# Performance work log

Hardware: AMD Instinct MI355X
Metric: run time of the kernel (lower is better)

The kernel has to match this reference:

```python
import jax, jax.numpy as jnp
import numpy as np

B, N, C_IN, T = 16, 1024, 16, 36
K, C_OUT = 3, 64


def setup_inputs() -> dict:
    key = jax.random.key(0)
    k1, k2, k3, k4 = jax.random.split(key, 4)
    x = jax.random.normal(k1, (B, N, C_IN, T), dtype=jnp.float32)
    spatial_attention = jax.random.uniform(k2, (B, N, N), dtype=jnp.float32)
    cheb = jax.random.normal(k3, (K, N, N), dtype=jnp.float32) * 0.1
    theta = jax.random.normal(k4, (K, C_IN, C_OUT), dtype=jnp.float32) * 0.1
    return {"x": x, "spatial_attention": spatial_attention, "cheb": cheb, "theta": theta}


def reference(x, spatial_attention, cheb, theta):
    # x: [B,N,C_in,T], spatial_attention: [B,N,N], cheb: [K,N,N], theta: [K,C_in,C_out]
    # Original: per (t,k): ((T_k * SAt).T @ x[..., t]) @ theta_k, summed over k, ReLU.
    # Compute attention-weighted adjacency ONCE (time-invariant), batch over all t.
    t_at = cheb[:, None, :, :] * spatial_attention[None]          # [K,B,N,N]
    # rhs[k,b,n,c,t] = sum_m t_at[k,b,m,n] * x[b,m,c,t]  (permute(0,2,1).matmul)
    rhs = jnp.einsum('kbmn,bmct->kbnct', t_at, x)                 # [K,B,N,C_in,T]
    out = jnp.einsum('kbnct,kco->bnot', rhs, theta)               # [B,N,C_out,T]
    return jax.nn.relu(out)
```

## Files before the change

kernel.cpp:

```cpp
#include <hip/hip_runtime.h>
#include <hip/hip_bf16.h>

#define NB 16
#define NN 1024
#define CIN 16
#define TT 36
#define KK 3
#define COUT 64
#define CT 576
#define KB 48

typedef __attribute__((ext_vector_type(8))) short bf16x8;
typedef __attribute__((ext_vector_type(4))) float f32x4;

__device__ __forceinline__ unsigned short f2bf(float f) {
    union { float f; unsigned int u; } v; v.f = f;
    unsigned int r = v.u + 0x7FFF + ((v.u >> 16) & 1);
    return (unsigned short)(r >> 16);
}

__global__ __launch_bounds__(256) void prep_a(const float* __restrict__ cheb,
                                              const float* __restrict__ sat,
                                              ushort* __restrict__ At,
                                              int n_base, int rows) {
    __shared__ ushort tile[64][68];
    const int ntiles = rows >> 6;
    const int k = blockIdx.y;
    const int n0 = n_base + (blockIdx.x % ntiles) * 64;
    const int m0 = (blockIdx.x / ntiles) * 64;
    const int tid = threadIdx.x;

    size_t goff[4];
    float4 cv[4], sv[4];
#pragma unroll
    for (int i = 0; i < 4; ++i) {
        int f = i * 256 + tid;
        goff[i] = (size_t)(m0 + (f >> 4)) * NN + n0 + ((f & 15) << 2);
        cv[i] = *(const float4*)(cheb + (size_t)k * NN * NN + goff[i]);
        sv[i] = *(const float4*)(sat + goff[i]);
    }
    for (int b = 0; b < 16; ++b) {
#pragma unroll
        for (int i = 0; i < 4; ++i) {
            int f = i * 256 + tid;
            ushort4 u;
            u.x = f2bf(cv[i].x * sv[i].x); u.y = f2bf(cv[i].y * sv[i].y);
            u.z = f2bf(cv[i].z * sv[i].z); u.w = f2bf(cv[i].w * sv[i].w);
            *(ushort4*)&tile[f >> 4][(f & 15) << 2] = u;
        }
        if (b < 15) {
            const float* sa = sat + (size_t)(b + 1) * NN * NN;
#pragma unroll
            for (int i = 0; i < 4; ++i) sv[i] = *(const float4*)(sa + goff[i]);
        }
        __syncthreads();
        ushort* outp = At + (size_t)(k * 16 + b) * rows * NN;
#pragma unroll
        for (int i = 0; i < 4; ++i) {
            int f = i * 256 + tid;
            int n = f >> 4, m4 = (f & 15) << 2;
            ushort4 u;
            u.x = tile[m4 + 0][n]; u.y = tile[m4 + 1][n];
            u.z = tile[m4 + 2][n]; u.w = tile[m4 + 3][n];
            *(ushort4*)(outp + (size_t)(n0 - n_base + n) * NN + m0 + m4) = u;
        }
        __syncthreads();
    }
}

__global__ __launch_bounds__(256) void prep_x(const float* __restrict__ x,
                                              ushort* __restrict__ Xt) {
    __shared__ ushort tile[64][68];
    const int b = blockIdx.y;
    const int m0 = (blockIdx.x & 15) * 64;
    const int c0 = (blockIdx.x >> 4) * 64;
    const int tid = threadIdx.x;
    const float* xb = x + (size_t)b * NN * CT;
#pragma unroll
    for (int i = 0; i < 4; ++i) {
        int f = i * 256 + tid;
        int mr = f >> 4, c4 = (f & 15) << 2;
        float4 v = *(const float4*)(xb + (size_t)(m0 + mr) * CT + c0 + c4);
        ushort4 u;
        u.x = f2bf(v.x); u.y = f2bf(v.y); u.z = f2bf(v.z); u.w = f2bf(v.w);
        *(ushort4*)&tile[mr][c4] = u;
    }
    __syncthreads();
    ushort* outp = Xt + (size_t)b * CT * NN;
#pragma unroll
    for (int i = 0; i < 4; ++i) {
        int f = i * 256 + tid;
        int n = f >> 4, m4 = (f & 15) << 2;
        int ctlin = c0 + n;
        int c = ctlin / 36, t = ctlin - 36 * c;
        int ctp = t * 16 + c;
        ushort4 u;
        u.x = tile[m4 + 0][n]; u.y = tile[m4 + 1][n];
        u.z = tile[m4 + 2][n]; u.w = tile[m4 + 3][n];
        *(ushort4*)(outp + (size_t)ctp * NN + m0 + m4) = u;
    }
}

__global__ __launch_bounds__(512) void gemm1(const ushort* __restrict__ At,
                                             const ushort* __restrict__ Xt,
                                             ushort* __restrict__ rhs2,
                                             int nsplit, int n_base, int rows) {
    __shared__ ushort lds[3 * 320 * 64];
    const int tid = threadIdx.x;
    const int y = blockIdx.y;
    const int b = y / 3, k = y - 3 * b;
    const int l = k * 16 + b;
    const int ntiles = rows >> 7;
    const int nt = blockIdx.x % ntiles;
    const int ctt = blockIdx.x / ntiles;
    const int nloc0 = nt * 128;
    const int ct0 = ctt * 192;
    const ushort* Ab = At + ((size_t)l * (nsplit ? rows : NN) + nloc0) * NN;
    const ushort* Bb = Xt + (size_t)b * CT * NN + (size_t)ct0 * NN;

    const int srow = tid >> 3;
    const int schunk = tid & 7;
    const int swz = schunk ^ (srow & 7);
    const ushort* a_src0 = Ab + (size_t)srow * NN + swz * 8;
    const ushort* b_src0 = Bb + (size_t)srow * NN + swz * 8;

    auto STAGE = [&](int kt, int p) {
        const int mk = kt * 64;
        ushort* base = lds + p * (320 * 64);
        const ushort* as = a_src0 + mk;
        const ushort* bs = b_src0 + mk;
#pragma unroll
        for (int i = 0; i < 2; ++i)
            __builtin_amdgcn_global_load_lds(
                (const __attribute__((address_space(1))) void*)(as + (size_t)i * 64 * NN),
                (__attribute__((address_space(3))) void*)(base + (tid + i * 512) * 8), 16, 0, 0);
#pragma unroll
        for (int i = 0; i < 3; ++i)
            __builtin_amdgcn_global_load_lds(
                (const __attribute__((address_space(1))) void*)(bs + (size_t)i * 64 * NN),
                (__attribute__((address_space(3))) void*)(base + 128 * 64 + (tid + i * 512) * 8), 16, 0, 0);
    };

    const int w = tid >> 6, lane = tid & 63;
    const int wr = w >> 2, wc = w & 3;
    const int lrow = lane & 15, quad = lane >> 4;
    const int koff0 = ((quad ^ (lrow & 7)) << 3);
    f32x4 acc[4][3] = {};

    STAGE(0, 0);
    STAGE(1, 1);
    asm volatile("s_waitcnt vmcnt(5)\n\ts_barrier" ::: "memory");

    for (int kt = 0; kt < 16; ++kt) {
        if (kt + 2 < 16)
            STAGE(kt + 2, (kt + 2) % 3);
        const ushort* bufA = lds + (kt % 3) * (320 * 64);
        const ushort* bufB = bufA + 128 * 64;
#pragma unroll
        for (int kp = 0; kp < 2; ++kp) {
            const int koff = koff0 ^ (kp << 5);
            bf16x8 af[4], bfr[3];
#pragma unroll
            for (int mi = 0; mi < 4; ++mi)
                af[mi] = *(const bf16x8*)&bufA[(wr * 64 + mi * 16 + lrow) * 64 + koff];
#pragma unroll
            for (int ni = 0; ni < 3; ++ni)
                bfr[ni] = *(const bf16x8*)&bufB[(wc * 48 + ni * 16 + lrow) * 64 + koff];
            __builtin_amdgcn_s_setprio(1);
#pragma unroll
            for (int mi = 0; mi < 4; ++mi)
#pragma unroll
                for (int ni = 0; ni < 3; ++ni)
                    acc[mi][ni] = __builtin_amdgcn_mfma_f32_16x16x32_bf16(
                        af[mi], bfr[ni], acc[mi][ni], 0, 0, 0);
            __builtin_amdgcn_s_setprio(0);
        }
        if (kt + 2 < 16)
            asm volatile("s_waitcnt vmcnt(5)\n\ts_barrier" ::: "memory");
        else if (kt + 1 < 16)
            asm volatile("s_waitcnt vmcnt(0)\n\ts_barrier" ::: "memory");
        else
            asm volatile("s_barrier" ::: "memory");
    }

    ushort* cs = lds;
#pragma unroll
    for (int mi = 0; mi < 4; ++mi)
#pragma unroll
        for (int ni = 0; ni < 3; ++ni)
#pragma unroll
            for (int r = 0; r < 4; ++r)
                cs[(wr * 64 + mi * 16 + quad * 4 + r) * 200 + wc * 48 + ni * 16 + lrow] =
                    f2bf(acc[mi][ni][r]);
    __syncthreads();

    for (int f = tid; f < 1536; f += 512) {
        int n = f / 12, tl = f - 12 * (f / 12);
        int t = ctt * 12 + tl;
        uint4 v0 = *(const uint4*)&cs[n * 200 + tl * 16];
        uint4 v1 = *(const uint4*)&cs[n * 200 + tl * 16 + 8];
        size_t g = (((size_t)b * NN + n_base + nloc0 + n) * 36 + t) * 48 + k * 16;
        *(uint4*)(rhs2 + g) = v0;
        *(uint4*)(rhs2 + g + 8) = v1;
    }
}

__global__ __launch_bounds__(256) void apply_mfma2(const ushort* __restrict__ rhs2,
                                                   const float* __restrict__ theta,
                                                   float* __restrict__ out) {
    __shared__ ushort thT[64 * 72];
    __shared__ float ostage[4][64 * 36];
    const int tid = threadIdx.x;
    for (int f = tid; f < 64 * 64; f += 256) {
        int o = f >> 6, kc = f & 63;
        thT[o * 72 + kc] = f2bf((kc < 48) ? theta[kc * 64 + o] : 0.f);
    }
    __syncthreads();
    const int w = tid >> 6, lane = tid & 63;
    const int lrow = lane & 15, quad = lane >> 4;

    bf16x8 a[4][2];
#pragma unroll
    for (int mi = 0; mi < 4; ++mi)
#pragma unroll
        for (int kc = 0; kc < 2; ++kc)
            a[mi][kc] = *(const bf16x8*)&thT[(mi * 16 + lrow) * 72 + kc * 32 + quad * 8];

    float* ost = &ostage[w][0];
    for (int j = 0; j < 4; ++j) {
        const int bn = blockIdx.x * 16 + w * 4 + j;
        const ushort* rrow = rhs2 + (size_t)bn * (36 * 48);
        f32x4 acc[4][3] = {};
#pragma unroll
        for (int ni = 0; ni < 3; ++ni)
#pragma unroll
            for (int kc = 0; kc < 2; ++kc) {
                bf16x8 bf = *(const bf16x8*)(rrow + (ni * 16 + lrow) * 48 + kc * 32 + quad * 8);
#pragma unroll
                for (int mi = 0; mi < 4; ++mi)
                    acc[mi][ni] = __builtin_amdgcn_mfma_f32_16x16x32_bf16(
                        a[mi][kc], bf, acc[mi][ni], 0, 0, 0);
            }
#pragma unroll
        for (int mi = 0; mi < 4; ++mi)
#pragma unroll
            for (int ni = 0; ni < 3; ++ni)
#pragma unroll
                for (int r = 0; r < 4; ++r) {
                    int t = ni * 16 + lrow;
                    if (t < 36)
                        ost[(mi * 16 + quad * 4 + r) * 36 + t] = fmaxf(acc[mi][ni][r], 0.f);
                }
        asm volatile("s_waitcnt lgkmcnt(0)" ::: "memory");
        float* ob = out + (size_t)bn * (COUT * TT);
#pragma unroll
        for (int q = 0; q < 9; ++q) {
            int f = q * 64 + lane;
            *(float4*)&ob[f * 4] = *(const float4*)&ost[f * 4];
        }
    }
}

__global__ __launch_bounds__(256) void naive_fused(const float* __restrict__ x,
                                                   const float* __restrict__ sat,
                                                   const float* __restrict__ cheb,
                                                   const float* __restrict__ theta,
                                                   float* __restrict__ out) {
    __shared__ float wgt[3][1024];
    __shared__ float rs[3][576];
    const int tid = threadIdx.x;
    const int n = blockIdx.x, b = blockIdx.y;
    for (int f = tid; f < 3 * 1024; f += 256) {
        int k = f >> 10, m = f & 1023;
        wgt[k][m] = cheb[(size_t)k * NN * NN + (size_t)m * NN + n] *
                    sat[(size_t)b * NN * NN + (size_t)m * NN + n];
    }
    __syncthreads();
    float a0[3] = {}, a1[3] = {}, a2[3] = {};
    const float* xb = x + (size_t)b * NN * CT;
    for (int m = 0; m < 1024; ++m) {
        const float* xr = xb + (size_t)m * CT;
        float x0 = xr[tid];
        float x1 = xr[256 + tid];
        float x2 = (tid < 64) ? xr[512 + tid] : 0.f;
#pragma unroll
        for (int k = 0; k < 3; ++k) {
            float wm = wgt[k][m];
            a0[k] += wm * x0; a1[k] += wm * x1; a2[k] += wm * x2;
        }
    }
#pragma unroll
    for (int k = 0; k < 3; ++k) {
        rs[k][tid] = a0[k];
        rs[k][256 + tid] = a1[k];
        if (tid < 64) rs[k][512 + tid] = a2[k];
    }
    __syncthreads();
    const int o = tid >> 2, tg = tid & 3;
    float oa[9] = {};
    for (int kc = 0; kc < 48; ++kc) {
        int k = kc >> 4, c = kc & 15;
        float th = theta[kc * 64 + o];
        const float* rp = &rs[k][c * TT + tg * 9];
#pragma unroll
        for (int j = 0; j < 9; ++j) oa[j] += th * rp[j];
    }
    float* ob = out + ((size_t)b * NN + n) * (COUT * TT);
#pragma unroll
    for (int j = 0; j < 9; ++j)
        ob[o * TT + tg * 9 + j] = fmaxf(oa[j], 0.f);
}

extern "C" void kernel_launch(void* const* d_in, const int* in_sizes, int n_in,
                              void* d_out, int out_size, void* d_ws, size_t ws_size,
                              hipStream_t stream) {
    const float* x     = (const float*)d_in[0];
    const float* sat   = (const float*)d_in[1];
    const float* cheb  = (const float*)d_in[2];
    const float* theta = (const float*)d_in[3];
    float* out = (float*)d_out;

    const size_t RHS2 = (size_t)NB * NN * 36 * 48;
    const size_t XT   = (size_t)NB * CT * NN;
    const size_t ATF  = (size_t)KB * NN * NN;
    const size_t ATNS = (size_t)KB * 512 * NN;
    const size_t needA     = (RHS2 + XT + ATF) * 2;
    const size_t needSplit = (RHS2 + XT + ATNS) * 2;

    ushort* rhs2 = (ushort*)d_ws;
    ushort* Xt   = rhs2 + RHS2;
    ushort* At   = Xt + XT;

    if (ws_size >= needA) {
        prep_x<<<dim3(144, NB), 256, 0, stream>>>(x, Xt);
        prep_a<<<dim3(256, KK), 256, 0, stream>>>(cheb, sat, At, 0, 1024);
        gemm1<<<dim3(24, KB), 512, 0, stream>>>(At, Xt, rhs2, 0, 0, 1024);
        apply_mfma2<<<dim3(NB * NN / 16), 256, 0, stream>>>(rhs2, theta, out);
    } else if (ws_size >= needSplit) {
        prep_x<<<dim3(144, NB), 256, 0, stream>>>(x, Xt);
        for (int half = 0; half < 2; ++half) {
            int nb = half * 512;
            prep_a<<<dim3(128, KK), 256, 0, stream>>>(cheb, sat, At, nb, 512);
            gemm1<<<dim3(12, KB), 512, 0, stream>>>(At, Xt, rhs2, 1, nb, 512);
        }
        apply_mfma2<<<dim3(NB * NN / 16), 256, 0, stream>>>(rhs2, theta, out);
    } else {
        naive_fused<<<dim3(NN, NB), 256, 0, stream>>>(x, sat, cheb, theta, out);
    }
}
```

Measured before the change: 384.6 us.

## Fuse all three Chebyshev orders into one gemm1 block to reuse X tiles

Each gemm1 block now handles all K=3 adjacency matrices for one batch, using a 64-row tile per k, so each staged X tile feeds three times as many MFMAs. This cuts redundant global loads of Xt, which were previously repeated per k. The epilogue is also rewritten as a per-wave LDS staging that writes contiguous 48-wide k-interleaved rows to rhs2, dropping the block-wide __syncthreads. The trade-off is more LDS (3x384x64 bf16 per block) and more accumulator registers, which may reduce occupancy.

```diff
diff --git a/kernel.cpp b/kernel.cpp
--- a/kernel.cpp
+++ b/kernel.cpp
@@ -105,103 +105,108 @@
                                              const ushort* __restrict__ Xt,
                                              ushort* __restrict__ rhs2,
                                              int nsplit, int n_base, int rows) {
-    __shared__ ushort lds[3 * 320 * 64];
-    const int tid = threadIdx.x;
-    const int y = blockIdx.y;
-    const int b = y / 3, k = y - 3 * b;
-    const int l = k * 16 + b;
-    const int ntiles = rows >> 7;
+    __shared__ ushort lds[3 * 384 * 64];
+    const int tid = threadIdx.x;
+    const int b = blockIdx.y;
+    const int ntiles = rows >> 6;
     const int nt = blockIdx.x % ntiles;
     const int ctt = blockIdx.x / ntiles;
-    const int nloc0 = nt * 128;
+    const int nloc0 = nt * 64;
     const int ct0 = ctt * 192;
-    const ushort* Ab = At + ((size_t)l * (nsplit ? rows : NN) + nloc0) * NN;
-    const ushort* Bb = Xt + (size_t)b * CT * NN + (size_t)ct0 * NN;
-
-    const int srow = tid >> 3;
-    const int schunk = tid & 7;
+    const int atrows = nsplit ? rows : NN;
+
+    const int srow = tid >> 3, schunk = tid & 7;
     const int swz = schunk ^ (srow & 7);
-    const ushort* a_src0 = Ab + (size_t)srow * NN + swz * 8;
-    const ushort* b_src0 = Bb + (size_t)srow * NN + swz * 8;
+    const ushort* a_src[3];
+#pragma unroll
+    for (int k = 0; k < 3; ++k)
+        a_src[k] = At + ((size_t)(k * 16 + b) * atrows + nloc0 + srow) * NN + swz * 8;
+    const ushort* b_src = Xt + (size_t)b * CT * NN + (size_t)(ct0 + srow) * NN + swz * 8;
 
     auto STAGE = [&](int kt, int p) {
         const int mk = kt * 64;
-        ushort* base = lds + p * (320 * 64);
-        const ushort* as = a_src0 + mk;
-        const ushort* bs = b_src0 + mk;
-#pragma unroll
-        for (int i = 0; i < 2; ++i)
+        ushort* base = lds + p * (384 * 64);
+#pragma unroll
+        for (int k = 0; k < 3; ++k)
             __builtin_amdgcn_global_load_lds(
-                (const __attribute__((address_space(1))) void*)(as + (size_t)i * 64 * NN),
-                (__attribute__((address_space(3))) void*)(base + (tid + i * 512) * 8), 16, 0, 0);
+                (const __attribute__((address_space(1))) void*)(a_src[k] + mk),
+                (__attribute__((address_space(3))) void*)(base + k * 4096 + tid * 8), 16, 0, 0);
 #pragma unroll
         for (int i = 0; i < 3; ++i)
             __builtin_amdgcn_global_load_lds(
-                (const __attribute__((address_space(1))) void*)(bs + (size_t)i * 64 * NN),
-                (__attribute__((address_space(3))) void*)(base + 128 * 64 + (tid + i * 512) * 8), 16, 0, 0);
+                (const __attribute__((address_space(1))) void*)(b_src + (size_t)i * 64 * NN + mk),
+                (__attribute__((address_space(3))) void*)(base + 3 * 4096 + (tid + i * 512) * 8), 16, 0, 0);
     };
 
     const int w = tid >> 6, lane = tid & 63;
     const int wr = w >> 2, wc = w & 3;
     const int lrow = lane & 15, quad = lane >> 4;
-    const int koff0 = ((quad ^ (lrow & 7)) << 3);
-    f32x4 acc[4][3] = {};
+    const int s3 = lrow & 7;
+    f32x4 acc[3][2][3] = {};
 
     STAGE(0, 0);
     STAGE(1, 1);
-    asm volatile("s_waitcnt vmcnt(5)\n\ts_barrier" ::: "memory");
+    asm volatile("s_waitcnt vmcnt(6)\n\ts_barrier" ::: "memory");
 
     for (int kt = 0; kt < 16; ++kt) {
         if (kt + 2 < 16)
             STAGE(kt + 2, (kt + 2) % 3);
-        const ushort* bufA = lds + (kt % 3) * (320 * 64);
-        const ushort* bufB = bufA + 128 * 64;
+        const ushort* bufA = lds + (kt % 3) * (384 * 64);
+        const ushort* bufB = bufA + 3 * 4096;
 #pragma unroll
         for (int kp = 0; kp < 2; ++kp) {
-            const int koff = koff0 ^ (kp << 5);
-            bf16x8 af[4], bfr[3];
-#pragma unroll
-            for (int mi = 0; mi < 4; ++mi)
-                af[mi] = *(const bf16x8*)&bufA[(wr * 64 + mi * 16 + lrow) * 64 + koff];
+            const int koff = (((kp * 4 + quad) ^ s3) << 3);
+            bf16x8 af[3][2], bfr[3];
+#pragma unroll
+            for (int k = 0; k < 3; ++k)
+#pragma unroll
+                for (int mi = 0; mi < 2; ++mi)
+                    af[k][mi] = *(const bf16x8*)&bufA[k * 4096 + (wr * 32 + mi * 16 + lrow) * 64 + koff];
 #pragma unroll
             for (int ni = 0; ni < 3; ++ni)
                 bfr[ni] = *(const bf16x8*)&bufB[(wc * 48 + ni * 16 + lrow) * 64 + koff];
             __builtin_amdgcn_s_setprio(1);
 #pragma unroll
-            for (int mi = 0; mi < 4; ++mi)
-#pragma unroll
-                for (int ni = 0; ni < 3; ++ni)
-                    acc[mi][ni] = __builtin_amdgcn_mfma_f32_16x16x32_bf16(
-                        af[mi], bfr[ni], acc[mi][ni], 0, 0, 0);
+            for (int k = 0; k < 3; ++k)
+#pragma unroll
+                for (int mi = 0; mi < 2; ++mi)
+#pragma unroll
+                    for (int ni = 0; ni < 3; ++ni)
+                        acc[k][mi][ni] = __builtin_amdgcn_mfma_f32_16x16x32_bf16(
+                            af[k][mi], bfr[ni], acc[k][mi][ni], 0, 0, 0);
             __builtin_amdgcn_s_setprio(0);
         }
         if (kt + 2 < 16)
-            asm volatile("s_waitcnt vmcnt(5)\n\ts_barrier" ::: "memory");
+            asm volatile("s_waitcnt vmcnt(6)\n\ts_barrier" ::: "memory");
         else if (kt + 1 < 16)
             asm volatile("s_waitcnt vmcnt(0)\n\ts_barrier" ::: "memory");
         else
             asm volatile("s_barrier" ::: "memory");
     }
 
-    ushort* cs = lds;
-#pragma unroll
-    for (int mi = 0; mi < 4; ++mi)
-#pragma unroll
-        for (int ni = 0; ni < 3; ++ni)
-#pragma unroll
-            for (int r = 0; r < 4; ++r)
-                cs[(wr * 64 + mi * 16 + quad * 4 + r) * 200 + wc * 48 + ni * 16 + lrow] =
-                    f2bf(acc[mi][ni][r]);
-    __syncthreads();
-
-    for (int f = tid; f < 1536; f += 512) {
-        int n = f / 12, tl = f - 12 * (f / 12);
-        int t = ctt * 12 + tl;
-        uint4 v0 = *(const uint4*)&cs[n * 200 + tl * 16];
-        uint4 v1 = *(const uint4*)&cs[n * 200 + tl * 16 + 8];
-        size_t g = (((size_t)b * NN + n_base + nloc0 + n) * 36 + t) * 48 + k * 16;
-        *(uint4*)(rhs2 + g) = v0;
-        *(uint4*)(rhs2 + g + 8) = v1;
+    ushort* sc = lds + w * 4608;
+#pragma unroll
+    for (int k = 0; k < 3; ++k)
+#pragma unroll
+        for (int mi = 0; mi < 2; ++mi)
+#pragma unroll
+            for (int ni = 0; ni < 3; ++ni)
+#pragma unroll
+                for (int r = 0; r < 4; ++r)
+                    sc[((mi * 16 + quad * 4 + r) * 3 + ni) * 48 + k * 16 + lrow] =
+                        f2bf(acc[k][mi][ni][r]);
+    asm volatile("s_waitcnt lgkmcnt(0)" ::: "memory");
+    const int n_g0 = n_base + nloc0 + wr * 32;
+    const int t_g0 = ctt * 12 + wc * 3;
+#pragma unroll
+    for (int i = 0; i < 9; ++i) {
+        int seg = i * 64 + lane;
+        int off = seg * 8;
+        int nl = off / 144;
+        int rem = off - nl * 144;
+        int tl = rem / 48, kcol = rem - tl * 48;
+        size_t g = (((size_t)b * NN + n_g0 + nl) * 36 + (t_g0 + tl)) * 48 + kcol;
+        *(uint4*)(rhs2 + g) = *(const uint4*)&sc[off];
     }
 }
 
@@ -334,14 +339,14 @@
     if (ws_size >= needA) {
         prep_x<<<dim3(144, NB), 256, 0, stream>>>(x, Xt);
         prep_a<<<dim3(256, KK), 256, 0, stream>>>(cheb, sat, At, 0, 1024);
-        gemm1<<<dim3(24, KB), 512, 0, stream>>>(At, Xt, rhs2, 0, 0, 1024);
+        gemm1<<<dim3(48, NB), 512, 0, stream>>>(At, Xt, rhs2, 0, 0, 1024);
         apply_mfma2<<<dim3(NB * NN / 16), 256, 0, stream>>>(rhs2, theta, out);
     } else if (ws_size >= needSplit) {
         prep_x<<<dim3(144, NB), 256, 0, stream>>>(x, Xt);
         for (int half = 0; half < 2; ++half) {
             int nb = half * 512;
             prep_a<<<dim3(128, KK), 256, 0, stream>>>(cheb, sat, At, nb, 512);
-            gemm1<<<dim3(12, KB), 512, 0, stream>>>(At, Xt, rhs2, 1, nb, 512);
+            gemm1<<<dim3(24, NB), 512, 0, stream>>>(At, Xt, rhs2, 1, nb, 512);
         }
         apply_mfma2<<<dim3(NB * NN / 16), 256, 0, stream>>>(rhs2, theta, out);
     } else {
```

New measurement: 376.6 us. 1.02x faster.
